# Performance work log

Hardware: AMD Instinct MI355X
Metric: run time of the kernel (lower is better)

The kernel has to match this reference:

```python
import jax, jax.numpy as jnp
import numpy as np

B, T, D, G, E, V = 32, 1024, 512, 256, 8, 8192


def setup_inputs() -> dict:
    key = jax.random.key(0)
    k1, k2, k3, k4, k5 = jax.random.split(key, 5)
    return {
        "gate_features": jax.random.normal(k1, (B, G), dtype=jnp.float32),
        "input_features": jax.random.normal(k2, (B, T, D), dtype=jnp.float32),
        "Wg": jax.random.normal(k3, (G, E), dtype=jnp.float32) * 0.02,
        "bg": jnp.zeros((E,), dtype=jnp.float32),
        "We": jax.random.normal(k4, (E, D, V), dtype=jnp.float32) * 0.02,
        "be": jnp.zeros((E, V), dtype=jnp.float32),
        "target_ids": jax.random.randint(k5, (B, T), 0, V, dtype=jnp.int64),
    }


def reference(gate_features, input_features, Wg, bg, We, be, target_ids):
    # ---- Router: linear gate -> softmax probs -> top-1 assignment ----
    router_logits = gate_features @ Wg + bg            # [B, E]
    probs = jax.nn.softmax(router_logits, axis=-1)     # [B, E]
    assignments = jnp.argmax(router_logits, axis=-1)   # [B]

    # ---- Dispatch: gather each sample's expert parameters ----
    W_sel = We[assignments]                            # [B, D, V]
    b_sel = be[assignments]                            # [B, V]

    # ---- Expert compute: linear LM head + cross-entropy loss ----
    logits = jnp.einsum("btd,bdv->btv", input_features, W_sel) + b_sel[:, None, :]
    logp = jax.nn.log_softmax(logits, axis=-1)         # [B, T, V]
    nll = -jnp.take_along_axis(logp, target_ids[..., None], axis=-1)[..., 0]  # [B, T]
    ce_per_sample = nll.mean(axis=-1)                  # [B]

    # ---- Combine: total_loss = sum over experts of per-expert mean loss ----
    sums = jax.ops.segment_sum(ce_per_sample, assignments, num_segments=E)   # [E]
    counts = jax.ops.segment_sum(jnp.ones_like(ce_per_sample), assignments, num_segments=E)
    loss_per_expert = jnp.where(counts > 0, sums / jnp.maximum(counts, 1.0), 0.0)
    total_loss = loss_per_expert.sum()

    return total_loss, assignments, probs
```

## Files before the change

### kernel.cpp

```cpp
#include <hip/hip_runtime.h>

#define NB 32
#define NT 1024
#define ND 512
#define NG 256
#define NE 8
#define NV 8192
#define NROW (NB * NT)

#define XBF_BYTES   (33554432)
#define WT_BYTES    (67108864)
#define PSUM_BYTES  (8388608)
#define TL_BYTES    (131072)

#define BM2 256
#define BN2 256
#define NCT (NV / BN2)

typedef float f32x4 __attribute__((ext_vector_type(4)));
typedef __bf16 bf16x8 __attribute__((ext_vector_type(8)));
typedef unsigned int u32_g __attribute__((address_space(1)));
typedef unsigned int u32_l __attribute__((address_space(3)));
typedef unsigned short ushort_t;

__device__ __forceinline__ void g2l16(void* lds, const void* g) {
    __builtin_amdgcn_global_load_lds((const u32_g*)g, (u32_l*)lds, 16, 0, 0);
}

__device__ __forceinline__ unsigned short f2bf(float f) {
    unsigned int u = __float_as_uint(f);
    unsigned int r = (u + 0x7fffu + ((u >> 16) & 1u)) >> 16;
    return (unsigned short)r;
}

__global__ void k_router(const float* __restrict__ gate, const float* __restrict__ Wg,
                         const float* __restrict__ bg, float* __restrict__ out,
                         int* __restrict__ assign, int* __restrict__ counts) {
    __shared__ float lg[NB][NE];
    __shared__ int lam[NB];
    int tid = threadIdx.x;
    int b = tid >> 3, e = tid & 7;
    float acc = bg[e];
    const float* gr = gate + b * NG;
    for (int g = 0; g < NG; ++g) acc = fmaf(gr[g], Wg[g * NE + e], acc);
    lg[b][e] = acc;
    __syncthreads();
    if (tid < NB) {
        float mx = lg[tid][0]; int am = 0;
        for (int j = 1; j < NE; ++j) { float v = lg[tid][j]; if (v > mx) { mx = v; am = j; } }
        float den = 0.f, ex[NE];
        for (int j = 0; j < NE; ++j) { ex[j] = __expf(lg[tid][j] - mx); den += ex[j]; }
        float inv = 1.f / den;
        for (int j = 0; j < NE; ++j) out[1 + NB + tid * NE + j] = ex[j] * inv;
        out[1 + tid] = (float)am;
        assign[tid] = am;
        lam[tid] = am;
    }
    __syncthreads();
    if (tid == 0) {
        int c[NE] = {0,0,0,0,0,0,0,0};
        for (int i = 0; i < NB; ++i) c[lam[i]]++;
        for (int j = 0; j < NE; ++j) counts[j] = c[j];
        out[0] = 0.f;
    }
}

__global__ void k_convx(const float4* __restrict__ in, ushort_t* __restrict__ out, int n4) {
    int i = blockIdx.x * blockDim.x + threadIdx.x;
    int stride = gridDim.x * blockDim.x;
    for (; i < n4; i += stride) {
        float4 v = in[i];
        ushort4 o;
        o.x = f2bf(v.x); o.y = f2bf(v.y); o.z = f2bf(v.z); o.w = f2bf(v.w);
        ((ushort4*)out)[i] = o;
    }
}

__global__ void k_transw(const float* __restrict__ We, ushort_t* __restrict__ Wt) {
    __shared__ float tile[32][33];
    int e = blockIdx.z, d0 = blockIdx.y * 32, v0 = blockIdx.x * 32;
    int tx = threadIdx.x & 31, ty = threadIdx.x >> 5;
    const float* src = We + (size_t)e * ND * NV;
    for (int j = 0; j < 4; ++j)
        tile[ty + j * 8][tx] = src[(size_t)(d0 + ty + j * 8) * NV + v0 + tx];
    __syncthreads();
    ushort_t* dst = Wt + (size_t)e * NV * ND;
    for (int j = 0; j < 4; ++j)
        dst[(size_t)(v0 + ty + j * 8) * ND + d0 + tx] = f2bf(tile[tx][ty + j * 8]);
}


#define BAR_MID() do { \
    asm volatile("" ::: "memory"); \
    __builtin_amdgcn_s_barrier(); \
    asm volatile("s_waitcnt lgkmcnt(0)" ::: "memory"); \
    __builtin_amdgcn_sched_barrier(0); } while (0)

#define BAR_END() do { \
    asm volatile("" ::: "memory"); \
    __builtin_amdgcn_s_barrier(); \
    asm volatile("" ::: "memory"); } while (0)

#define MFMA_QUAD(MH, NH) do { \
    __builtin_amdgcn_s_setprio(1); \
    _Pragma("unroll") \
    for (int m_ = 0; m_ < 4; ++m_) \
      _Pragma("unroll") \
      for (int n_ = 0; n_ < 2; ++n_) \
        _Pragma("unroll") \
        for (int ks_ = 0; ks_ < 2; ++ks_) \
          acc[(MH) * 4 + m_][(NH) * 2 + n_] = __builtin_amdgcn_mfma_f32_16x16x32_bf16( \
              af[m_][ks_], bfr[(NH) * 2 + n_][ks_], acc[(MH) * 4 + m_][(NH) * 2 + n_], 0, 0, 0); \
    __builtin_amdgcn_s_setprio(0); } while (0)

__global__ __launch_bounds__(512, 2)
void k_gemm(const ushort_t* __restrict__ Xbf, const ushort_t* __restrict__ Wtbf,
            const float* __restrict__ be, const int* __restrict__ assign,
            float* __restrict__ psum) {
    __shared__ alignas(16) char smem[135168];
    float* lws = (float*)(smem + 131072);

    const int tid  = threadIdx.x;
    const int wid  = tid >> 6, lane = tid & 63;
    const int q = lane >> 4, ln = lane & 15;
    const int wr = wid >> 2, wc = wid & 3;

    const int bid = blockIdx.x;
    const int wg  = ((bid & 7) << 9) | (bid >> 3);
    const int ct  = wg >> 7;
    const int rt  = wg & 127;
    const int e   = assign[rt >> 2];
    const size_t eV = (size_t)e * NV;

    const int rquo = tid >> 3;
    const int scol = ((tid & 7) ^ (rquo & 7)) << 3;
    const ushort_t* gA = Xbf + (size_t)(rt * BM2 + rquo) * ND + scol;
    const ushort_t* gB = Wtbf + (eV + ct * BN2 + rquo) * ND + scol;
    char* ldsW = smem + wid * 1024;
    const int axor = ln & 7;

    f32x4 acc[8][4];
#pragma unroll
    for (int i = 0; i < 8; ++i)
#pragma unroll
        for (int j = 0; j < 4; ++j) acc[i][j] = (f32x4){0.f, 0.f, 0.f, 0.f};

#define STA(KT, BP, H) do { \
    char* d_ = ldsW + (BP) * 65536 + (H) * 16384; \
    const ushort_t* g_ = gA + (size_t)(H) * 128 * ND + (KT) * 64; \
    g2l16(d_, g_); g2l16(d_ + 8192, g_ + (size_t)64 * ND); } while (0)

#define STB(KT, BP, H) do { \
    char* d_ = ldsW + (BP) * 65536 + 32768 + (H) * 16384; \
    const ushort_t* g_ = gB + (size_t)(H) * 128 * ND + (KT) * 64; \
    g2l16(d_, g_); g2l16(d_ + 8192, g_ + (size_t)64 * ND); } while (0)

#define RDA(BP, MF, KS) \
    (*(const bf16x8*)(smem + (BP) * 65536 + wr * 16384 + \
                      ((MF) * 16 + ln) * 128 + ((((KS) * 4 + q) ^ axor) << 4)))

#define RDB(BP, NF, KS) \
    (*(const bf16x8*)(smem + (BP) * 65536 + 32768 + (wc >> 1) * 16384 + \
                      (((wc & 1) * 64 + (NF) * 16 + ln) * 128) + ((((KS) * 4 + q) ^ axor) << 4)))

    STB(0, 0, 0); STB(0, 0, 1); STA(0, 0, 0); STA(0, 0, 1);
    STB(1, 1, 0); STB(1, 1, 1);
    asm volatile("s_waitcnt vmcnt(4)" ::: "memory");
    __builtin_amdgcn_s_barrier();
    asm volatile("" ::: "memory");

    bf16x8 af[4][2];
    bf16x8 bfr[4][2];

#pragma unroll
    for (int kt = 0; kt < 8; ++kt) {
        const int p = kt & 1, np = p ^ 1;

#pragma unroll
        for (int m = 0; m < 4; ++m) { af[m][0] = RDA(p, m, 0); af[m][1] = RDA(p, m, 1); }
#pragma unroll
        for (int n = 0; n < 2; ++n) { bfr[n][0] = RDB(p, n, 0); bfr[n][1] = RDB(p, n, 1); }
        if (kt < 7) STA(kt + 1, np, 0);
        BAR_MID();
        MFMA_QUAD(0, 0);
        BAR_END();

#pragma unroll
        for (int n = 0; n < 2; ++n) { bfr[2 + n][0] = RDB(p, 2 + n, 0); bfr[2 + n][1] = RDB(p, 2 + n, 1); }
        if (kt < 7) STA(kt + 1, np, 1);
        BAR_MID();
        MFMA_QUAD(0, 1);
        BAR_END();

#pragma unroll
        for (int m = 0; m < 4; ++m) { af[m][0] = RDA(p, 4 + m, 0); af[m][1] = RDA(p, 4 + m, 1); }
        if (kt < 6) STB(kt + 2, p, 0);
        BAR_MID();
        MFMA_QUAD(1, 1);
        BAR_END();

        if (kt < 6) STB(kt + 2, p, 1);
        BAR_MID();
        MFMA_QUAD(1, 0);
        if (kt < 6)       { asm volatile("s_waitcnt vmcnt(4)" ::: "memory"); }
        else if (kt == 6) { asm volatile("s_waitcnt vmcnt(0)" ::: "memory"); }
        BAR_END();
    }

    const float LOG2E = 1.44269504088896f;
    float partial[32];
#pragma unroll
    for (int i = 0; i < 32; ++i) partial[i] = 0.f;
#pragma unroll
    for (int nf = 0; nf < 4; ++nf) {
        int col = (ct << 8) + (wc << 6) + nf * 16 + ln;
        float eb = be[eV + col] * LOG2E;
#pragma unroll
        for (int mf = 0; mf < 8; ++mf)
#pragma unroll
            for (int r = 0; r < 4; ++r)
                partial[mf * 4 + r] += exp2f(fmaf(acc[mf][nf][r], LOG2E, eb));
    }
#pragma unroll
    for (int i = 0; i < 32; ++i) {
        float pv = partial[i];
        pv += __shfl_xor(pv, 1); pv += __shfl_xor(pv, 2);
        pv += __shfl_xor(pv, 4); pv += __shfl_xor(pv, 8);
        partial[i] = pv;
    }
    if (ln == 0) {
#pragma unroll
        for (int mf = 0; mf < 8; ++mf)
#pragma unroll
            for (int r = 0; r < 4; ++r)
                lws[wid * 128 + mf * 16 + q * 4 + r] = partial[mf * 4 + r];
    }
    __syncthreads();
    if (tid < 256) {
        int wrh = tid >> 7, idx = tid & 127;
        float s = lws[(wrh * 4 + 0) * 128 + idx] + lws[(wrh * 4 + 1) * 128 + idx]
                + lws[(wrh * 4 + 2) * 128 + idx] + lws[(wrh * 4 + 3) * 128 + idx];
        psum[(size_t)ct * NROW + rt * 256 + tid] = s;
    }
#undef STA
#undef STB
#undef RDA
#undef RDB
}

__global__ void k_target(const ushort_t* __restrict__ Xbf, const ushort_t* __restrict__ Wtbf,
                         const float* __restrict__ be, const int* __restrict__ assign,
                         const int* __restrict__ tgt, float* __restrict__ tl) {
    int wave = threadIdx.x >> 6, lane = threadIdx.x & 63;
    int wg = blockIdx.x * 4 + wave;
    int b = wg >> 10, t = wg & 1023;
    int e = assign[b];
    int id = tgt[b * NT + t];
    const bf16x8 xv = *(const bf16x8*)(Xbf + (size_t)(b * NT + t) * ND + lane * 8);
    const bf16x8 wv = *(const bf16x8*)(Wtbf + ((size_t)e * NV + id) * ND + lane * 8);
    float s = 0.f;
#pragma unroll
    for (int i = 0; i < 8; ++i) s = fmaf((float)xv[i], (float)wv[i], s);
    for (int off = 32; off; off >>= 1) s += __shfl_down(s, off);
    if (lane == 0) tl[b * NT + t] = s + be[(size_t)e * NV + id];
}

__global__ void k_loss(const float* __restrict__ psum, const float* __restrict__ tl,
                       float* __restrict__ nll) {
    int b = blockIdx.x, tid = threadIdx.x;
    float acc = 0.f;
#pragma unroll
    for (int j = 0; j < 4; ++j) {
        int t = j * 256 + tid;
        float s = 0.f;
        for (int ct = 0; ct < NCT; ++ct) s += psum[(size_t)ct * NROW + b * NT + t];
        acc += __logf(s) - tl[b * NT + t];
    }
    __shared__ float red[4];
    for (int off = 32; off; off >>= 1) acc += __shfl_down(acc, off);
    if ((tid & 63) == 0) red[tid >> 6] = acc;
    __syncthreads();
    if (tid == 0) nll[b] = red[0] + red[1] + red[2] + red[3];
}

__global__ void k_final(const float* __restrict__ nll_sum, const int* __restrict__ assign,
                        const int* __restrict__ counts, float* __restrict__ out) {
    int tid = threadIdx.x;
    float contrib = 0.f;
    if (tid < NB) {
        float ce = nll_sum[tid] * (1.0f / (float)NT);
        contrib = ce / (float)counts[assign[tid]];
    }
    for (int off = 32; off; off >>= 1) contrib += __shfl_down(contrib, off);
    if (tid == 0) out[0] = contrib;
}

extern "C" void kernel_launch(void* const* d_in, const int* in_sizes, int n_in,
                              void* d_out, int out_size, void* d_ws, size_t ws_size,
                              hipStream_t stream) {
    const float* gate = (const float*)d_in[0];
    const float* X    = (const float*)d_in[1];
    const float* Wg   = (const float*)d_in[2];
    const float* bg   = (const float*)d_in[3];
    const float* We   = (const float*)d_in[4];
    const float* be   = (const float*)d_in[5];
    const int*   tgt  = (const int*)d_in[6];
    float* out = (float*)d_out;

    char* ws = (char*)d_ws;
    ushort_t* Xbf  = (ushort_t*)ws;
    ushort_t* Wtbf = (ushort_t*)(ws + XBF_BYTES);
    float*    psum = (float*)(ws + XBF_BYTES + WT_BYTES);
    float*    tl   = (float*)(ws + XBF_BYTES + WT_BYTES + PSUM_BYTES);
    int*      assign = (int*)(ws + XBF_BYTES + WT_BYTES + PSUM_BYTES + TL_BYTES);
    int*      counts = assign + 32;
    float*    nll    = (float*)(assign + 64);

    k_router<<<1, 256, 0, stream>>>(gate, Wg, bg, out, assign, counts);
    k_convx<<<4096, 256, 0, stream>>>((const float4*)X, Xbf, NB * NT * ND / 4);
    k_transw<<<dim3(NV / 32, ND / 32, NE), 256, 0, stream>>>(We, Wtbf);
    k_gemm<<<(NROW / BM2) * (NV / BN2), 512, 0, stream>>>(Xbf, Wtbf, be, assign, psum);
    k_target<<<NB * NT / 4, 256, 0, stream>>>(Xbf, Wtbf, be, assign, tgt, tl);
    k_loss<<<NB, 256, 0, stream>>>(psum, tl, nll);
    k_final<<<1, 64, 0, stream>>>(nll, assign, counts, out);
}
```

Baseline: 599.4 us.

## Fuse router into convert, target logit into GEMM, final into loss; vectorize transpose

Moves the router into block 0 of the X conversion kernel, computes each row's target logit inside the GEMM epilogue by matching the column index against the target ID, and folds the final combine into the loss kernel through an atomicAdd. The weight transpose kernel now uses 64x64 tiles with float4 loads, swizzled LDS, and 16-byte bf16 stores. These changes cut kernel launches and the separate target-gather pass, and widen memory access in the transpose. In exchange the GEMM epilogue gains compare and conditional-store work plus extra LDS. The atomic order makes the loss sum non-deterministic, and out[0] being zeroed by block 0 of the convert kernel relies on stream ordering.

```diff
diff --git a/kernel.cpp b/kernel.cpp
--- a/kernel.cpp
+++ b/kernel.cpp
@@ -19,6 +19,7 @@
 
 typedef float f32x4 __attribute__((ext_vector_type(4)));
 typedef __bf16 bf16x8 __attribute__((ext_vector_type(8)));
+typedef unsigned short ushort8_v __attribute__((ext_vector_type(8)));
 typedef unsigned int u32_g __attribute__((address_space(1)));
 typedef unsigned int u32_l __attribute__((address_space(3)));
 typedef unsigned short ushort_t;
@@ -33,60 +34,75 @@
     return (unsigned short)r;
 }
 
-__global__ void k_router(const float* __restrict__ gate, const float* __restrict__ Wg,
-                         const float* __restrict__ bg, float* __restrict__ out,
-                         int* __restrict__ assign, int* __restrict__ counts) {
-    __shared__ float lg[NB][NE];
-    __shared__ int lam[NB];
+__global__ void k_convx(const float4* __restrict__ in, ushort_t* __restrict__ out4, int n4,
+                        const float* __restrict__ gate, const float* __restrict__ Wg,
+                        const float* __restrict__ bg, float* __restrict__ out,
+                        int* __restrict__ assign, int* __restrict__ counts) {
     int tid = threadIdx.x;
-    int b = tid >> 3, e = tid & 7;
-    float acc = bg[e];
-    const float* gr = gate + b * NG;
-    for (int g = 0; g < NG; ++g) acc = fmaf(gr[g], Wg[g * NE + e], acc);
-    lg[b][e] = acc;
-    __syncthreads();
-    if (tid < NB) {
-        float mx = lg[tid][0]; int am = 0;
-        for (int j = 1; j < NE; ++j) { float v = lg[tid][j]; if (v > mx) { mx = v; am = j; } }
-        float den = 0.f, ex[NE];
-        for (int j = 0; j < NE; ++j) { ex[j] = __expf(lg[tid][j] - mx); den += ex[j]; }
-        float inv = 1.f / den;
-        for (int j = 0; j < NE; ++j) out[1 + NB + tid * NE + j] = ex[j] * inv;
-        out[1 + tid] = (float)am;
-        assign[tid] = am;
-        lam[tid] = am;
-    }
-    __syncthreads();
-    if (tid == 0) {
-        int c[NE] = {0,0,0,0,0,0,0,0};
-        for (int i = 0; i < NB; ++i) c[lam[i]]++;
-        for (int j = 0; j < NE; ++j) counts[j] = c[j];
-        out[0] = 0.f;
-    }
-}
-
-__global__ void k_convx(const float4* __restrict__ in, ushort_t* __restrict__ out, int n4) {
-    int i = blockIdx.x * blockDim.x + threadIdx.x;
+    if (blockIdx.x == 0) {
+        __shared__ float lg[NB][NE];
+        __shared__ int lam[NB];
+        int b = tid >> 3, e = tid & 7;
+        float acc = bg[e];
+        const float* gr = gate + b * NG;
+        for (int g = 0; g < NG; ++g) acc = fmaf(gr[g], Wg[g * NE + e], acc);
+        lg[b][e] = acc;
+        __syncthreads();
+        if (tid < NB) {
+            float mx = lg[tid][0]; int am = 0;
+            for (int j = 1; j < NE; ++j) { float v = lg[tid][j]; if (v > mx) { mx = v; am = j; } }
+            float den = 0.f, ex[NE];
+            for (int j = 0; j < NE; ++j) { ex[j] = __expf(lg[tid][j] - mx); den += ex[j]; }
+            float inv = 1.f / den;
+            for (int j = 0; j < NE; ++j) out[1 + NB + tid * NE + j] = ex[j] * inv;
+            out[1 + tid] = (float)am;
+            assign[tid] = am;
+            lam[tid] = am;
+        }
+        __syncthreads();
+        if (tid == 0) {
+            int c[NE] = {0,0,0,0,0,0,0,0};
+            for (int i = 0; i < NB; ++i) c[lam[i]]++;
+            for (int j = 0; j < NE; ++j) counts[j] = c[j];
+            out[0] = 0.f;
+        }
+    }
+    int i = blockIdx.x * blockDim.x + tid;
     int stride = gridDim.x * blockDim.x;
     for (; i < n4; i += stride) {
         float4 v = in[i];
         ushort4 o;
         o.x = f2bf(v.x); o.y = f2bf(v.y); o.z = f2bf(v.z); o.w = f2bf(v.w);
-        ((ushort4*)out)[i] = o;
+        ((ushort4*)out4)[i] = o;
     }
 }
 
 __global__ void k_transw(const float* __restrict__ We, ushort_t* __restrict__ Wt) {
-    __shared__ float tile[32][33];
-    int e = blockIdx.z, d0 = blockIdx.y * 32, v0 = blockIdx.x * 32;
-    int tx = threadIdx.x & 31, ty = threadIdx.x >> 5;
-    const float* src = We + (size_t)e * ND * NV;
-    for (int j = 0; j < 4; ++j)
-        tile[ty + j * 8][tx] = src[(size_t)(d0 + ty + j * 8) * NV + v0 + tx];
+    __shared__ float tile[64][68];
+    int e = blockIdx.z, d0 = blockIdx.y * 64, v0 = blockIdx.x * 64;
+    int tid = threadIdx.x;
+    const float* src = We + (size_t)e * ND * NV + (size_t)d0 * NV + v0;
+    int dr = tid >> 4;
+    int c4 = tid & 15;
+#pragma unroll
+    for (int j = 0; j < 4; ++j) {
+        int d = dr + 16 * j;
+        float4 v = *(const float4*)(src + (size_t)d * NV + c4 * 4);
+        *(float4*)&tile[d][((c4 ^ (d >> 3)) & 15) * 4] = v;
+    }
     __syncthreads();
-    ushort_t* dst = Wt + (size_t)e * NV * ND;
-    for (int j = 0; j < 4; ++j)
-        dst[(size_t)(v0 + ty + j * 8) * ND + d0 + tx] = f2bf(tile[tx][ty + j * 8]);
+    ushort_t* dst = Wt + (size_t)e * NV * ND + (size_t)v0 * ND + d0;
+    int vr = tid >> 3;
+    int t8 = tid & 7;
+#pragma unroll
+    for (int j = 0; j < 2; ++j) {
+        int v = vr + 32 * j;
+        ushort8_v o;
+#pragma unroll
+        for (int i = 0; i < 8; ++i)
+            o[i] = f2bf(tile[t8 * 8 + i][(((v >> 2) ^ t8) & 15) * 4 + (v & 3)]);
+        *(ushort8_v*)(dst + (size_t)v * ND + t8 * 8) = o;
+    }
 }
 
 
@@ -116,9 +132,11 @@
 __global__ __launch_bounds__(512, 2)
 void k_gemm(const ushort_t* __restrict__ Xbf, const ushort_t* __restrict__ Wtbf,
             const float* __restrict__ be, const int* __restrict__ assign,
-            float* __restrict__ psum) {
-    __shared__ alignas(16) char smem[135168];
+            const int* __restrict__ tgt, float* __restrict__ psum,
+            float* __restrict__ tl) {
+    __shared__ alignas(16) char smem[136192];
     float* lws = (float*)(smem + 131072);
+    int*   lt  = (int*)(smem + 135168);
 
     const int tid  = threadIdx.x;
     const int wid  = tid >> 6, lane = tid & 63;
@@ -139,6 +157,8 @@
     char* ldsW = smem + wid * 1024;
     const int axor = ln & 7;
 
+    if (tid < 256) lt[tid] = tgt[rt * BM2 + tid];
+
     f32x4 acc[8][4];
 #pragma unroll
     for (int i = 0; i < 8; ++i)
@@ -208,18 +228,29 @@
     }
 
     const float LOG2E = 1.44269504088896f;
+    int tcv[8][4];
+#pragma unroll
+    for (int mf = 0; mf < 8; ++mf)
+#pragma unroll
+        for (int r = 0; r < 4; ++r)
+            tcv[mf][r] = lt[wr * 128 + mf * 16 + q * 4 + r];
+
     float partial[32];
 #pragma unroll
     for (int i = 0; i < 32; ++i) partial[i] = 0.f;
 #pragma unroll
     for (int nf = 0; nf < 4; ++nf) {
         int col = (ct << 8) + (wc << 6) + nf * 16 + ln;
-        float eb = be[eV + col] * LOG2E;
+        float br = be[eV + col];
+        float eb = br * LOG2E;
 #pragma unroll
         for (int mf = 0; mf < 8; ++mf)
 #pragma unroll
-            for (int r = 0; r < 4; ++r)
+            for (int r = 0; r < 4; ++r) {
                 partial[mf * 4 + r] += exp2f(fmaf(acc[mf][nf][r], LOG2E, eb));
+                if (col == tcv[mf][r])
+                    tl[rt * BM2 + wr * 128 + mf * 16 + q * 4 + r] = acc[mf][nf][r] + br;
+            }
     }
 #pragma unroll
     for (int i = 0; i < 32; ++i) {
@@ -248,25 +279,9 @@
 #undef RDB
 }
 
-__global__ void k_target(const ushort_t* __restrict__ Xbf, const ushort_t* __restrict__ Wtbf,
-                         const float* __restrict__ be, const int* __restrict__ assign,
-                         const int* __restrict__ tgt, float* __restrict__ tl) {
-    int wave = threadIdx.x >> 6, lane = threadIdx.x & 63;
-    int wg = blockIdx.x * 4 + wave;
-    int b = wg >> 10, t = wg & 1023;
-    int e = assign[b];
-    int id = tgt[b * NT + t];
-    const bf16x8 xv = *(const bf16x8*)(Xbf + (size_t)(b * NT + t) * ND + lane * 8);
-    const bf16x8 wv = *(const bf16x8*)(Wtbf + ((size_t)e * NV + id) * ND + lane * 8);
-    float s = 0.f;
-#pragma unroll
-    for (int i = 0; i < 8; ++i) s = fmaf((float)xv[i], (float)wv[i], s);
-    for (int off = 32; off; off >>= 1) s += __shfl_down(s, off);
-    if (lane == 0) tl[b * NT + t] = s + be[(size_t)e * NV + id];
-}
-
 __global__ void k_loss(const float* __restrict__ psum, const float* __restrict__ tl,
-                       float* __restrict__ nll) {
+                       const int* __restrict__ assign, const int* __restrict__ counts,
+                       float* __restrict__ out) {
     int b = blockIdx.x, tid = threadIdx.x;
     float acc = 0.f;
 #pragma unroll
@@ -280,19 +295,11 @@
     for (int off = 32; off; off >>= 1) acc += __shfl_down(acc, off);
     if ((tid & 63) == 0) red[tid >> 6] = acc;
     __syncthreads();
-    if (tid == 0) nll[b] = red[0] + red[1] + red[2] + red[3];
-}
-
-__global__ void k_final(const float* __restrict__ nll_sum, const int* __restrict__ assign,
-                        const int* __restrict__ counts, float* __restrict__ out) {
-    int tid = threadIdx.x;
-    float contrib = 0.f;
-    if (tid < NB) {
-        float ce = nll_sum[tid] * (1.0f / (float)NT);
-        contrib = ce / (float)counts[assign[tid]];
-    }
-    for (int off = 32; off; off >>= 1) contrib += __shfl_down(contrib, off);
-    if (tid == 0) out[0] = contrib;
+    if (tid == 0) {
+        float nb = red[0] + red[1] + red[2] + red[3];
+        float ce = nb * (1.0f / (float)NT);
+        atomicAdd(out, ce / (float)counts[assign[b]]);
+    }
 }
 
 extern "C" void kernel_launch(void* const* d_in, const int* in_sizes, int n_in,
@@ -314,13 +321,10 @@
     float*    tl   = (float*)(ws + XBF_BYTES + WT_BYTES + PSUM_BYTES);
     int*      assign = (int*)(ws + XBF_BYTES + WT_BYTES + PSUM_BYTES + TL_BYTES);
     int*      counts = assign + 32;
-    float*    nll    = (float*)(assign + 64);
-
-    k_router<<<1, 256, 0, stream>>>(gate, Wg, bg, out, assign, counts);
-    k_convx<<<4096, 256, 0, stream>>>((const float4*)X, Xbf, NB * NT * ND / 4);
-    k_transw<<<dim3(NV / 32, ND / 32, NE), 256, 0, stream>>>(We, Wtbf);
-    k_gemm<<<(NROW / BM2) * (NV / BN2), 512, 0, stream>>>(Xbf, Wtbf, be, assign, psum);
-    k_target<<<NB * NT / 4, 256, 0, stream>>>(Xbf, Wtbf, be, assign, tgt, tl);
-    k_loss<<<NB, 256, 0, stream>>>(psum, tl, nll);
-    k_final<<<1, 64, 0, stream>>>(nll, assign, counts, out);
-}
+
+    k_convx<<<4096, 256, 0, stream>>>((const float4*)X, Xbf, NB * NT * ND / 4,
+                                      gate, Wg, bg, out, assign, counts);
+    k_transw<<<dim3(NV / 64, ND / 64, NE), 256, 0, stream>>>(We, Wtbf);
+    k_gemm<<<(NROW / BM2) * (NV / BN2), 512, 0, stream>>>(Xbf, Wtbf, be, assign, tgt, psum, tl);
+    k_loss<<<NB, 256, 0, stream>>>(psum, tl, assign, counts, out);
+}
```

Result: no change. 608.4 us (+1.5%).
